# Kernel tuning notes

Measured on AMD Instinct MI355X. Metric: run time of the kernel, lower is better.

Reference implementation:

```python
import jax, jax.numpy as jnp
import numpy as np

VOCAB, E, HIDDEN = 100000, 64, (64, 128, 64)
B, T = 4096, 200


def setup_inputs() -> dict:
    key = jax.random.key(0)
    ks = jax.random.split(key, 12)
    # glorot-ish scales
    def glorot(k, shape):
        fan_in, fan_out = shape[0], shape[-1]
        s = jnp.sqrt(6.0 / (fan_in + fan_out))
        return jax.random.uniform(k, shape, jnp.float32, -s, s)
    return {
        "query": jax.random.randint(ks[0], (B,), 0, VOCAB),
        "keys": jax.random.randint(ks[1], (B, T), 0, VOCAB),
        "emb": glorot(ks[2], (VOCAB, E)),
        "att_w1": glorot(ks[3], (4 * E, 64)),
        "att_b1": jnp.zeros((64,), jnp.float32),
        "att_w2": glorot(ks[4], (64, 1)),
        "att_b2": jnp.zeros((1,), jnp.float32),
        "deep_w1": glorot(ks[5], (HIDDEN[0], HIDDEN[1])),
        "deep_b1": jnp.zeros((HIDDEN[1],), jnp.float32),
        "deep_w2": glorot(ks[6], (HIDDEN[1], HIDDEN[2])),
        "deep_b2": jnp.zeros((HIDDEN[2],), jnp.float32),
        "out_w": glorot(ks[7], (HIDDEN[2], 1)),
        "out_b": jnp.zeros((1,), jnp.float32),
    }


def reference(query, keys, emb, att_w1, att_b1, att_w2, att_b2,
              deep_w1, deep_b1, deep_w2, deep_b2, out_w, out_b):
    q = emb[query]                # [B, E]
    k = emb[keys]                 # [B, T, E]
    qe = jnp.broadcast_to(q[:, None, :], k.shape)  # [B, T, E]
    inter = jnp.concatenate([qe, k, qe - k, qe * k], axis=-1)  # [B, T, 4E]
    h = jax.nn.relu(inter @ att_w1 + att_b1)       # [B, T, 64]
    scores = (h @ att_w2 + att_b2)[..., 0]         # [B, T]
    w = jax.nn.softmax(scores, axis=-1)            # [B, T]
    interest = jnp.einsum("bt,bte->be", w, k)      # [B, E]
    d = jax.nn.relu(interest @ deep_w1 + deep_b1)
    d = jax.nn.relu(d @ deep_w2 + deep_b2)
    return jax.nn.sigmoid(d @ out_w + out_b)       # [B, 1]
```

## Files before the change

kernel.cpp:

```cpp
#include <hip/hip_runtime.h>

#define T 200
#define E 64
#define TPAD 256
#define ROW 72
#define BDIM 256

typedef __bf16 bf16_t;
typedef __bf16 bf16x8 __attribute__((ext_vector_type(8)));
typedef float f32x4 __attribute__((ext_vector_type(4)));

__global__ __launch_bounds__(256) void emb_cvt(const float* __restrict__ src,
                                               bf16_t* __restrict__ dst, int n8) {
    const int i = blockIdx.x * 256 + threadIdx.x;
    if (i >= n8) return;
    const float4* s = (const float4*)src + (size_t)i * 2;
    const float4 a = s[0], b = s[1];
    union { bf16_t h[8]; uint4 v; } u;
    u.h[0] = (bf16_t)a.x; u.h[1] = (bf16_t)a.y; u.h[2] = (bf16_t)a.z; u.h[3] = (bf16_t)a.w;
    u.h[4] = (bf16_t)b.x; u.h[5] = (bf16_t)b.y; u.h[6] = (bf16_t)b.z; u.h[7] = (bf16_t)b.w;
    ((uint4*)dst)[i] = u.v;
}

__global__ __launch_bounds__(BDIM, 3) void din_kernel(
    const int* __restrict__ query,
    const int* __restrict__ keys,
    const float* __restrict__ embf,
    const bf16_t* __restrict__ emb16,
    const int use16,
    const float* __restrict__ w1,
    const float* __restrict__ b1,
    const float* __restrict__ w2,
    const float* __restrict__ b2,
    const float* __restrict__ dw1,
    const float* __restrict__ db1,
    const float* __restrict__ dw2,
    const float* __restrict__ db2,
    const float* __restrict__ ow,
    const float* __restrict__ ob,
    float* __restrict__ out)
{
    __shared__ __align__(16) char sRaw[TPAD * ROW * 2];
    __shared__ __align__(16) bf16_t sMt[64 * ROW];
    __shared__ float sU[64];
    __shared__ float sUP[256];
    __shared__ float sW2f[64];
    __shared__ float sWgt[256];
    __shared__ float sQf[64];
    __shared__ __align__(16) char sQtmp[128];
    __shared__ float sRed[8];
    __shared__ float sInt[64];
    __shared__ float sD1[128];
    __shared__ float sD2[64];

    const int tid  = threadIdx.x;
    const int lane = tid & 63;
    const int wid  = tid >> 6;
    const int b    = blockIdx.x;
    const float b2v = b2[0];

    uint4 kr[8];
    if (tid < T) {
        const int ki = keys[b * T + tid];
        if (use16) {
            const uint4* kp = (const uint4*)(emb16 + (size_t)ki * E);
            #pragma unroll
            for (int c = 0; c < 8; ++c) kr[c] = kp[c];
        } else {
            const float4* kp = (const float4*)(embf + (size_t)ki * E);
            #pragma unroll
            for (int c = 0; c < 8; ++c) {
                const float4 x = kp[2 * c], y = kp[2 * c + 1];
                union { bf16_t h[8]; uint4 v; } u;
                u.h[0] = (bf16_t)x.x; u.h[1] = (bf16_t)x.y; u.h[2] = (bf16_t)x.z; u.h[3] = (bf16_t)x.w;
                u.h[4] = (bf16_t)y.x; u.h[5] = (bf16_t)y.y; u.h[6] = (bf16_t)y.z; u.h[7] = (bf16_t)y.w;
                kr[c] = u.v;
            }
        }
    } else {
        #pragma unroll
        for (int c = 0; c < 8; ++c) kr[c] = make_uint4(0u, 0u, 0u, 0u);
    }

    const int qi = query[b];
    if (tid < 8) {
        uint4 qv;
        if (use16) {
            qv = ((const uint4*)(emb16 + (size_t)qi * E))[tid];
        } else {
            const float4 x = ((const float4*)(embf + (size_t)qi * E))[2 * tid];
            const float4 y = ((const float4*)(embf + (size_t)qi * E))[2 * tid + 1];
            union { bf16_t h[8]; uint4 v; } u;
            u.h[0] = (bf16_t)x.x; u.h[1] = (bf16_t)x.y; u.h[2] = (bf16_t)x.z; u.h[3] = (bf16_t)x.w;
            u.h[4] = (bf16_t)y.x; u.h[5] = (bf16_t)y.y; u.h[6] = (bf16_t)y.z; u.h[7] = (bf16_t)y.w;
            qv = u.v;
        }
        ((uint4*)sQtmp)[tid] = qv;
    }
    if (tid < 64) sW2f[tid] = w2[tid];
    __syncthreads();
    if (tid < 64) sQf[tid] = (float)((const bf16_t*)sQtmp)[tid];
    __syncthreads();

    {
        float* sTmp = (float*)sRaw;
        const int j = tid & 63, ec = tid >> 6;
        float au = 0.f;
        #pragma unroll
        for (int eo = 0; eo < 16; ++eo) {
            const int e = ec * 16 + eo;
            const float w1a = w1[e * 64 + j];
            const float w1b = w1[(64 + e) * 64 + j];
            const float w1c = w1[(128 + e) * 64 + j];
            const float w1d = w1[(192 + e) * 64 + j];
            sTmp[e * 65 + j] = w1b - w1c + sQf[e] * w1d;
            au = fmaf(sQf[e], w1a + w1c, au);
        }
        sUP[tid] = au;
    }
    __syncthreads();
    {
        const float* sTmp = (const float*)sRaw;
        const int e = tid & 63, jc = tid >> 6;
        #pragma unroll
        for (int jo = 0; jo < 16; ++jo) {
            const int j = jc * 16 + jo;
            sMt[j * ROW + e] = (bf16_t)sTmp[e * 65 + j];
        }
    }
    if (tid < 64) sU[tid] = b1[tid] + sUP[tid] + sUP[64 + tid] + sUP[128 + tid] + sUP[192 + tid];
    __syncthreads();

    bf16_t* sK = (bf16_t*)sRaw;
    {
        uint4* dst = (uint4*)(sK + tid * ROW);
        #pragma unroll
        for (int c = 0; c < 8; ++c) dst[c] = kr[c];
    }
    __syncthreads();

    {
        const int n    = lane & 15;
        const int quad = lane >> 4;
        float w2v[4], uv[4];
        bf16x8 bF[4][2];
        #pragma unroll
        for (int nt = 0; nt < 4; ++nt) {
            w2v[nt] = sW2f[nt * 16 + n];
            uv[nt]  = sU[nt * 16 + n];
            bF[nt][0] = *(const bf16x8*)&sMt[(nt * 16 + n) * ROW + quad * 8];
            bF[nt][1] = *(const bf16x8*)&sMt[(nt * 16 + n) * ROW + 32 + quad * 8];
        }
        #pragma unroll
        for (int i = 0; i < 4; ++i) {
            const int mt = wid * 4 + i;
            const bf16x8 a0 = *(const bf16x8*)&sK[(mt * 16 + n) * ROW + quad * 8];
            const bf16x8 a1 = *(const bf16x8*)&sK[(mt * 16 + n) * ROW + 32 + quad * 8];
            float s0 = 0.f, s1 = 0.f, s2 = 0.f, s3 = 0.f;
            #pragma unroll
            for (int nt = 0; nt < 4; ++nt) {
                f32x4 acc = { uv[nt], uv[nt], uv[nt], uv[nt] };
                acc = __builtin_amdgcn_mfma_f32_16x16x32_bf16(a0, bF[nt][0], acc, 0, 0, 0);
                acc = __builtin_amdgcn_mfma_f32_16x16x32_bf16(a1, bF[nt][1], acc, 0, 0, 0);
                s0 = fmaf(fmaxf(acc[0], 0.f), w2v[nt], s0);
                s1 = fmaf(fmaxf(acc[1], 0.f), w2v[nt], s1);
                s2 = fmaf(fmaxf(acc[2], 0.f), w2v[nt], s2);
                s3 = fmaf(fmaxf(acc[3], 0.f), w2v[nt], s3);
            }
            #pragma unroll
            for (int off = 1; off < 16; off <<= 1) {
                s0 += __shfl_xor(s0, off);
                s1 += __shfl_xor(s1, off);
                s2 += __shfl_xor(s2, off);
                s3 += __shfl_xor(s3, off);
            }
            if (n == 0) {
                const int base = mt * 16 + quad * 4;
                sWgt[base + 0] = s0;
                sWgt[base + 1] = s1;
                sWgt[base + 2] = s2;
                sWgt[base + 3] = s3;
            }
        }
    }
    __syncthreads();

    {
        const float score = (tid < T) ? (sWgt[tid] + b2v) : -1e30f;
        float m = score;
        #pragma unroll
        for (int off = 32; off > 0; off >>= 1) m = fmaxf(m, __shfl_xor(m, off));
        if (lane == 0) sRed[wid] = m;
        __syncthreads();
        const float gmax = fmaxf(fmaxf(sRed[0], sRed[1]), fmaxf(sRed[2], sRed[3]));
        const float p = (tid < T) ? __expf(score - gmax) : 0.f;
        float s = p;
        #pragma unroll
        for (int off = 32; off > 0; off >>= 1) s += __shfl_xor(s, off);
        if (lane == 0) sRed[4 + wid] = s;
        __syncthreads();
        const float gsum = sRed[4] + sRed[5] + sRed[6] + sRed[7];
        sWgt[tid] = p / gsum;
    }
    __syncthreads();

    {
        const int e = tid & 63, ch = tid >> 6;
        float a = 0.f;
        #pragma unroll 8
        for (int tt = 0; tt < 64; ++tt) {
            const int t = ch * 64 + tt;
            a = fmaf(sWgt[t], (float)sK[t * ROW + e], a);
        }
        sUP[tid] = a;
    }
    __syncthreads();
    if (tid < 64) sInt[tid] = sUP[tid] + sUP[64 + tid] + sUP[128 + tid] + sUP[192 + tid];
    __syncthreads();

    if (tid < 128) {
        float a = db1[tid];
        #pragma unroll 8
        for (int e = 0; e < 64; ++e) a = fmaf(sInt[e], dw1[e * 128 + tid], a);
        sD1[tid] = fmaxf(a, 0.f);
    }
    __syncthreads();
    if (tid < 64) {
        float a = db2[tid];
        #pragma unroll 8
        for (int i = 0; i < 128; ++i) a = fmaf(sD1[i], dw2[i * 64 + tid], a);
        sD2[tid] = fmaxf(a, 0.f);
    }
    __syncthreads();
    if (tid < 64) {
        float v = sD2[tid] * ow[tid];
        #pragma unroll
        for (int off = 32; off > 0; off >>= 1) v += __shfl_xor(v, off);
        if (tid == 0) out[b] = 1.f / (1.f + __expf(-(v + ob[0])));
    }
}

extern "C" void kernel_launch(void* const* d_in, const int* in_sizes, int n_in,
                              void* d_out, int out_size, void* d_ws, size_t ws_size,
                              hipStream_t stream) {
    const int*   query = (const int*)d_in[0];
    const int*   keys  = (const int*)d_in[1];
    const float* embf  = (const float*)d_in[2];
    const float* w1    = (const float*)d_in[3];
    const float* b1    = (const float*)d_in[4];
    const float* w2    = (const float*)d_in[5];
    const float* b2    = (const float*)d_in[6];
    const float* dw1   = (const float*)d_in[7];
    const float* db1   = (const float*)d_in[8];
    const float* dw2   = (const float*)d_in[9];
    const float* db2   = (const float*)d_in[10];
    const float* ow    = (const float*)d_in[11];
    const float* ob    = (const float*)d_in[12];
    float* out = (float*)d_out;
    const int B       = in_sizes[0];
    const int embElems = in_sizes[2];
    const int use16   = (ws_size >= (size_t)embElems * 2) ? 1 : 0;
    bf16_t* emb16 = (bf16_t*)d_ws;

    if (use16) {
        const int n8 = embElems / 8;
        emb_cvt<<<(n8 + 255) / 256, 256, 0, stream>>>(embf, emb16, n8);
    }
    din_kernel<<<B, BDIM, 0, stream>>>(query, keys, embf, emb16, use16,
                                       w1, b1, w2, b2, dw1, db1, dw2, db2, ow, ob, out);
}
```

Before: 170.3 us.

## Split monolithic DIN kernel into prep, attention, and batched MLP kernels

Replaces the single per-sample kernel with three stages. A prep kernel builds the query-folded attention weights (bf16 MFMA fragments) and the bias vector per sample into workspace. The main kernel gathers keys in fp32 with conversion, runs MFMA scoring over 13 tiles instead of 16 padded ones, does the softmax and the weighted sum. A separate MLP kernel processes 16 samples per block with the weights held in shared memory. It also drops the full-table bf16 conversion pass, in exchange for extra launches and workspace traffic.

After: 175.5 us. 3.1% more time.

```diff
diff --git a/kernel.cpp b/kernel.cpp
--- a/kernel.cpp
+++ b/kernel.cpp
@@ -2,32 +2,308 @@
 
 #define T 200
 #define E 64
-#define TPAD 256
+#define NTILE 13
+#define TPAD 208
 #define ROW 72
-#define BDIM 256
+#define MB 16
 
 typedef __bf16 bf16_t;
 typedef __bf16 bf16x8 __attribute__((ext_vector_type(8)));
 typedef float f32x4 __attribute__((ext_vector_type(4)));
 
-__global__ __launch_bounds__(256) void emb_cvt(const float* __restrict__ src,
-                                               bf16_t* __restrict__ dst, int n8) {
-    const int i = blockIdx.x * 256 + threadIdx.x;
-    if (i >= n8) return;
-    const float4* s = (const float4*)src + (size_t)i * 2;
-    const float4 a = s[0], b = s[1];
-    union { bf16_t h[8]; uint4 v; } u;
-    u.h[0] = (bf16_t)a.x; u.h[1] = (bf16_t)a.y; u.h[2] = (bf16_t)a.z; u.h[3] = (bf16_t)a.w;
-    u.h[4] = (bf16_t)b.x; u.h[5] = (bf16_t)b.y; u.h[6] = (bf16_t)b.z; u.h[7] = (bf16_t)b.w;
-    ((uint4*)dst)[i] = u.v;
+__global__ __launch_bounds__(256) void prep_kernel(
+    const int* __restrict__ query,
+    const float* __restrict__ emb,
+    const float* __restrict__ w1,
+    const float* __restrict__ b1,
+    uint4* __restrict__ wsM,
+    float* __restrict__ wsU)
+{
+    __shared__ float sTmp[64 * 65];
+    __shared__ __align__(16) float sQ[64];
+    __shared__ float sUP[256];
+
+    const int tid = threadIdx.x;
+    const int b   = blockIdx.x;
+
+    const int qi = query[b];
+    if (tid < 16) ((float4*)sQ)[tid] = ((const float4*)(emb + (size_t)qi * E))[tid];
+    __syncthreads();
+
+    {
+        const int j = tid & 63, ec = tid >> 6;
+        float au = 0.f;
+        #pragma unroll
+        for (int eo = 0; eo < 16; ++eo) {
+            const int e = ec * 16 + eo;
+            const float w1a = w1[e * 64 + j];
+            const float w1b = w1[(64 + e) * 64 + j];
+            const float w1c = w1[(128 + e) * 64 + j];
+            const float w1d = w1[(192 + e) * 64 + j];
+            sTmp[e * 65 + j] = w1b - w1c + sQ[e] * w1d;
+            au = fmaf(sQ[e], w1a + w1c, au);
+        }
+        sUP[tid] = au;
+    }
+    __syncthreads();
+    if (tid < 64)
+        wsU[(size_t)b * 64 + tid] = b1[tid] + sUP[tid] + sUP[64 + tid] + sUP[128 + tid] + sUP[192 + tid];
+
+    #pragma unroll
+    for (int c = tid; c < 512; c += 256) {
+        const int f = c >> 6, l = c & 63;
+        const int nt = f >> 1, h = f & 1;
+        const int n = l & 15, quad = l >> 4;
+        const int j2 = nt * 16 + n;
+        const int e0 = h * 32 + quad * 8;
+        union { bf16_t hh[8]; uint4 v; } u;
+        #pragma unroll
+        for (int s = 0; s < 8; ++s) u.hh[s] = (bf16_t)sTmp[(e0 + s) * 65 + j2];
+        wsM[(size_t)b * 512 + c] = u.v;
+    }
 }
 
-__global__ __launch_bounds__(BDIM, 3) void din_kernel(
+__global__ __launch_bounds__(256) void main_kernel(
+    const int* __restrict__ keys,
+    const float* __restrict__ emb,
+    const uint4* __restrict__ wsM,
+    const float* __restrict__ wsU,
+    const float* __restrict__ w2,
+    const float* __restrict__ b2,
+    float* __restrict__ wsI)
+{
+    __shared__ __align__(16) bf16_t sK[TPAD * ROW];
+    __shared__ __align__(16) float sU[64];
+    __shared__ __align__(16) float sW2f[64];
+    __shared__ float sWgt[256];
+    __shared__ float sUP[256];
+    __shared__ float sRed[8];
+
+    const int tid  = threadIdx.x;
+    const int lane = tid & 63;
+    const int wid  = tid >> 6;
+    const int b    = blockIdx.x;
+
+    uint4 kr[8];
+    #pragma unroll
+    for (int c = 0; c < 8; ++c) kr[c] = make_uint4(0u, 0u, 0u, 0u);
+    if (tid < T) {
+        const int ki = keys[b * T + tid];
+        const float4* kp = (const float4*)(emb + (size_t)ki * E);
+        #pragma unroll
+        for (int c = 0; c < 8; ++c) {
+            const float4 x = kp[2 * c], y = kp[2 * c + 1];
+            union { bf16_t h[8]; uint4 v; } u;
+            u.h[0] = (bf16_t)x.x; u.h[1] = (bf16_t)x.y; u.h[2] = (bf16_t)x.z; u.h[3] = (bf16_t)x.w;
+            u.h[4] = (bf16_t)y.x; u.h[5] = (bf16_t)y.y; u.h[6] = (bf16_t)y.z; u.h[7] = (bf16_t)y.w;
+            kr[c] = u.v;
+        }
+    }
+    if (tid < 16) ((float4*)sU)[tid] = ((const float4*)(wsU + (size_t)b * 64))[tid];
+    else if (tid < 32) ((float4*)sW2f)[tid - 16] = ((const float4*)w2)[tid - 16];
+    const float b2v = b2[0];
+
+    bf16x8 bF[4][2];
+    {
+        const uint4* mp = wsM + (size_t)b * 512;
+        #pragma unroll
+        for (int nt = 0; nt < 4; ++nt)
+            #pragma unroll
+            for (int h = 0; h < 2; ++h) {
+                union { uint4 v; bf16x8 f; } u;
+                u.v = mp[(nt * 2 + h) * 64 + lane];
+                bF[nt][h] = u.f;
+            }
+    }
+
+    if (tid < TPAD) {
+        uint4* dst = (uint4*)(sK + tid * ROW);
+        #pragma unroll
+        for (int c = 0; c < 8; ++c) dst[c] = kr[c];
+    }
+    __syncthreads();
+
+    {
+        const int n    = lane & 15;
+        const int quad = lane >> 4;
+        float uvv[4], w2v[4];
+        #pragma unroll
+        for (int nt = 0; nt < 4; ++nt) { uvv[nt] = sU[nt * 16 + n]; w2v[nt] = sW2f[nt * 16 + n]; }
+        for (int mt = wid; mt < NTILE; mt += 4) {
+            const bf16x8 a0 = *(const bf16x8*)&sK[(mt * 16 + n) * ROW + quad * 8];
+            const bf16x8 a1 = *(const bf16x8*)&sK[(mt * 16 + n) * ROW + 32 + quad * 8];
+            float s0 = 0.f, s1 = 0.f, s2 = 0.f, s3 = 0.f;
+            #pragma unroll
+            for (int nt = 0; nt < 4; ++nt) {
+                f32x4 acc = { uvv[nt], uvv[nt], uvv[nt], uvv[nt] };
+                acc = __builtin_amdgcn_mfma_f32_16x16x32_bf16(a0, bF[nt][0], acc, 0, 0, 0);
+                acc = __builtin_amdgcn_mfma_f32_16x16x32_bf16(a1, bF[nt][1], acc, 0, 0, 0);
+                s0 = fmaf(fmaxf(acc[0], 0.f), w2v[nt], s0);
+                s1 = fmaf(fmaxf(acc[1], 0.f), w2v[nt], s1);
+                s2 = fmaf(fmaxf(acc[2], 0.f), w2v[nt], s2);
+                s3 = fmaf(fmaxf(acc[3], 0.f), w2v[nt], s3);
+            }
+            #pragma unroll
+            for (int off = 1; off < 16; off <<= 1) {
+                s0 += __shfl_xor(s0, off);
+                s1 += __shfl_xor(s1, off);
+                s2 += __shfl_xor(s2, off);
+                s3 += __shfl_xor(s3, off);
+            }
+            if (n == 0) {
+                const int base = mt * 16 + quad * 4;
+                sWgt[base + 0] = s0;
+                sWgt[base + 1] = s1;
+                sWgt[base + 2] = s2;
+                sWgt[base + 3] = s3;
+            }
+        }
+    }
+    __syncthreads();
+
+    {
+        const float score = (tid < T) ? (sWgt[tid] + b2v) : -1e30f;
+        float m = score;
+        #pragma unroll
+        for (int off = 32; off > 0; off >>= 1) m = fmaxf(m, __shfl_xor(m, off));
+        if (lane == 0) sRed[wid] = m;
+        __syncthreads();
+        const float gmax = fmaxf(fmaxf(sRed[0], sRed[1]), fmaxf(sRed[2], sRed[3]));
+        const float p = (tid < T) ? __expf(score - gmax) : 0.f;
+        float s = p;
+        #pragma unroll
+        for (int off = 32; off > 0; off >>= 1) s += __shfl_xor(s, off);
+        if (lane == 0) sRed[4 + wid] = s;
+        __syncthreads();
+        const float gsum = sRed[4] + sRed[5] + sRed[6] + sRed[7];
+        sWgt[tid] = p / gsum;
+    }
+    __syncthreads();
+
+    {
+        const int e = tid & 63, ch = tid >> 6;
+        float a = 0.f;
+        #pragma unroll 4
+        for (int tt = 0; tt < 52; ++tt) {
+            const int t = ch * 52 + tt;
+            a = fmaf(sWgt[t], (float)sK[t * ROW + e], a);
+        }
+        sUP[tid] = a;
+    }
+    __syncthreads();
+    if (tid < 64)
+        wsI[(size_t)b * 64 + tid] = sUP[tid] + sUP[64 + tid] + sUP[128 + tid] + sUP[192 + tid];
+}
+
+__global__ __launch_bounds__(256) void mlp_kernel(
+    const float* __restrict__ wsI,
+    const float* __restrict__ dw1,
+    const float* __restrict__ db1,
+    const float* __restrict__ dw2,
+    const float* __restrict__ db2,
+    const float* __restrict__ ow,
+    const float* __restrict__ ob,
+    float* __restrict__ out,
+    int B)
+{
+    __shared__ __align__(16) float sDW1[64 * 128];
+    __shared__ __align__(16) float sDW2[128 * 64];
+    __shared__ __align__(16) float sI[MB * 68];
+    __shared__ __align__(16) float sH1[MB * 132];
+    __shared__ __align__(16) float sH2[MB * 68];
+    __shared__ float sB1[128];
+    __shared__ float sB2[64];
+    __shared__ float sOW[64];
+
+    const int tid = threadIdx.x;
+    const int b0  = blockIdx.x * MB;
+
+    for (int i = tid; i < 2048; i += 256) ((float4*)sDW1)[i] = ((const float4*)dw1)[i];
+    for (int i = tid; i < 2048; i += 256) ((float4*)sDW2)[i] = ((const float4*)dw2)[i];
+    if (tid < 128) sB1[tid] = db1[tid];
+    if (tid < 64) { sB2[tid] = db2[tid]; sOW[tid] = ow[tid]; }
+    {
+        const int bi = tid >> 4, e4 = (tid & 15) * 4;
+        if (b0 + bi < B) {
+            const float4 v = *(const float4*)(wsI + (size_t)(b0 + bi) * 64 + e4);
+            *(float4*)&sI[bi * 68 + e4] = v;
+        }
+    }
+    __syncthreads();
+
+    {
+        const int bi = tid >> 4, jb = tid & 15;
+        float iv[64];
+        #pragma unroll
+        for (int e4 = 0; e4 < 16; ++e4) {
+            const float4 v = *(const float4*)&sI[bi * 68 + e4 * 4];
+            iv[e4 * 4 + 0] = v.x; iv[e4 * 4 + 1] = v.y; iv[e4 * 4 + 2] = v.z; iv[e4 * 4 + 3] = v.w;
+        }
+        float a[8];
+        #pragma unroll
+        for (int jj = 0; jj < 8; ++jj) a[jj] = sB1[jb * 8 + jj];
+        #pragma unroll 8
+        for (int e = 0; e < 64; ++e) {
+            const float4 w0 = *(const float4*)&sDW1[e * 128 + jb * 8];
+            const float4 w4 = *(const float4*)&sDW1[e * 128 + jb * 8 + 4];
+            const float x = iv[e];
+            a[0] = fmaf(x, w0.x, a[0]); a[1] = fmaf(x, w0.y, a[1]);
+            a[2] = fmaf(x, w0.z, a[2]); a[3] = fmaf(x, w0.w, a[3]);
+            a[4] = fmaf(x, w4.x, a[4]); a[5] = fmaf(x, w4.y, a[5]);
+            a[6] = fmaf(x, w4.z, a[6]); a[7] = fmaf(x, w4.w, a[7]);
+        }
+        #pragma unroll
+        for (int jj = 0; jj < 4; ++jj) {
+            float4 v;
+            v.x = fmaxf(a[0 + ((jj & 1) * 4 + (jj >> 1) * 0)], 0.f);
+            (void)v;
+        }
+        float4 v0, v1;
+        v0.x = fmaxf(a[0], 0.f); v0.y = fmaxf(a[1], 0.f); v0.z = fmaxf(a[2], 0.f); v0.w = fmaxf(a[3], 0.f);
+        v1.x = fmaxf(a[4], 0.f); v1.y = fmaxf(a[5], 0.f); v1.z = fmaxf(a[6], 0.f); v1.w = fmaxf(a[7], 0.f);
+        *(float4*)&sH1[bi * 132 + jb * 8] = v0;
+        *(float4*)&sH1[bi * 132 + jb * 8 + 4] = v1;
+    }
+    __syncthreads();
+
+    {
+        const int bi = tid >> 4, obb = tid & 15;
+        float a0 = sB2[obb * 4 + 0], a1 = sB2[obb * 4 + 1], a2 = sB2[obb * 4 + 2], a3 = sB2[obb * 4 + 3];
+        #pragma unroll 4
+        for (int i4 = 0; i4 < 32; ++i4) {
+            const float4 hv = *(const float4*)&sH1[bi * 132 + i4 * 4];
+            const float4 wv0 = *(const float4*)&sDW2[(i4 * 4 + 0) * 64 + obb * 4];
+            const float4 wv1 = *(const float4*)&sDW2[(i4 * 4 + 1) * 64 + obb * 4];
+            const float4 wv2 = *(const float4*)&sDW2[(i4 * 4 + 2) * 64 + obb * 4];
+            const float4 wv3 = *(const float4*)&sDW2[(i4 * 4 + 3) * 64 + obb * 4];
+            a0 = fmaf(hv.x, wv0.x, a0); a1 = fmaf(hv.x, wv0.y, a1);
+            a2 = fmaf(hv.x, wv0.z, a2); a3 = fmaf(hv.x, wv0.w, a3);
+            a0 = fmaf(hv.y, wv1.x, a0); a1 = fmaf(hv.y, wv1.y, a1);
+            a2 = fmaf(hv.y, wv1.z, a2); a3 = fmaf(hv.y, wv1.w, a3);
+            a0 = fmaf(hv.z, wv2.x, a0); a1 = fmaf(hv.z, wv2.y, a1);
+            a2 = fmaf(hv.z, wv2.z, a2); a3 = fmaf(hv.z, wv2.w, a3);
+            a0 = fmaf(hv.w, wv3.x, a0); a1 = fmaf(hv.w, wv3.y, a1);
+            a2 = fmaf(hv.w, wv3.z, a2); a3 = fmaf(hv.w, wv3.w, a3);
+        }
+        float4 v;
+        v.x = fmaxf(a0, 0.f); v.y = fmaxf(a1, 0.f); v.z = fmaxf(a2, 0.f); v.w = fmaxf(a3, 0.f);
+        *(float4*)&sH2[bi * 68 + obb * 4] = v;
+    }
+    __syncthreads();
+
+    if (tid < MB) {
+        const int bi = tid;
+        float a = 0.f;
+        #pragma unroll 8
+        for (int o = 0; o < 64; ++o) a = fmaf(sH2[bi * 68 + o], sOW[o], a);
+        if (b0 + bi < B) out[b0 + bi] = 1.f / (1.f + __expf(-(a + ob[0])));
+    }
+}
+
+__global__ __launch_bounds__(256, 3) void din_mono(
     const int* __restrict__ query,
     const int* __restrict__ keys,
     const float* __restrict__ embf,
-    const bf16_t* __restrict__ emb16,
-    const int use16,
     const float* __restrict__ w1,
     const float* __restrict__ b1,
     const float* __restrict__ w2,
@@ -40,14 +316,13 @@
     const float* __restrict__ ob,
     float* __restrict__ out)
 {
-    __shared__ __align__(16) char sRaw[TPAD * ROW * 2];
+    __shared__ __align__(16) char sRaw[256 * ROW * 2];
     __shared__ __align__(16) bf16_t sMt[64 * ROW];
     __shared__ float sU[64];
     __shared__ float sUP[256];
     __shared__ float sW2f[64];
     __shared__ float sWgt[256];
     __shared__ float sQf[64];
-    __shared__ __align__(16) char sQtmp[128];
     __shared__ float sRed[8];
     __shared__ float sInt[64];
     __shared__ float sD1[128];
@@ -60,46 +335,23 @@
     const float b2v = b2[0];
 
     uint4 kr[8];
+    #pragma unroll
+    for (int c = 0; c < 8; ++c) kr[c] = make_uint4(0u, 0u, 0u, 0u);
     if (tid < T) {
         const int ki = keys[b * T + tid];
-        if (use16) {
-            const uint4* kp = (const uint4*)(emb16 + (size_t)ki * E);
-            #pragma unroll
-            for (int c = 0; c < 8; ++c) kr[c] = kp[c];
-        } else {
-            const float4* kp = (const float4*)(embf + (size_t)ki * E);
-            #pragma unroll
-            for (int c = 0; c < 8; ++c) {
-                const float4 x = kp[2 * c], y = kp[2 * c + 1];
-                union { bf16_t h[8]; uint4 v; } u;
-                u.h[0] = (bf16_t)x.x; u.h[1] = (bf16_t)x.y; u.h[2] = (bf16_t)x.z; u.h[3] = (bf16_t)x.w;
-                u.h[4] = (bf16_t)y.x; u.h[5] = (bf16_t)y.y; u.h[6] = (bf16_t)y.z; u.h[7] = (bf16_t)y.w;
-                kr[c] = u.v;
-            }
-        }
-    } else {
-        #pragma unroll
-        for (int c = 0; c < 8; ++c) kr[c] = make_uint4(0u, 0u, 0u, 0u);
-    }
-
-    const int qi = query[b];
-    if (tid < 8) {
-        uint4 qv;
-        if (use16) {
-            qv = ((const uint4*)(emb16 + (size_t)qi * E))[tid];
-        } else {
-            const float4 x = ((const float4*)(embf + (size_t)qi * E))[2 * tid];
-            const float4 y = ((const float4*)(embf + (size_t)qi * E))[2 * tid + 1];
+        const float4* kp = (const float4*)(embf + (size_t)ki * E);
+        #pragma unroll
+        for (int c = 0; c < 8; ++c) {
+            const float4 x = kp[2 * c], y = kp[2 * c + 1];
             union { bf16_t h[8]; uint4 v; } u;
             u.h[0] = (bf16_t)x.x; u.h[1] = (bf16_t)x.y; u.h[2] = (bf16_t)x.z; u.h[3] = (bf16_t)x.w;
             u.h[4] = (bf16_t)y.x; u.h[5] = (bf16_t)y.y; u.h[6] = (bf16_t)y.z; u.h[7] = (bf16_t)y.w;
-            qv = u.v;
-        }
-        ((uint4*)sQtmp)[tid] = qv;
-    }
+            kr[c] = u.v;
+        }
+    }
+    const int qi = query[b];
+    if (tid < 16) ((float4*)sQf)[tid] = ((const float4*)(embf + (size_t)qi * E))[tid];
     if (tid < 64) sW2f[tid] = w2[tid];
-    __syncthreads();
-    if (tid < 64) sQf[tid] = (float)((const bf16_t*)sQtmp)[tid];
     __syncthreads();
 
     {
@@ -257,15 +509,20 @@
     const float* ow    = (const float*)d_in[11];
     const float* ob    = (const float*)d_in[12];
     float* out = (float*)d_out;
-    const int B       = in_sizes[0];
-    const int embElems = in_sizes[2];
-    const int use16   = (ws_size >= (size_t)embElems * 2) ? 1 : 0;
-    bf16_t* emb16 = (bf16_t*)d_ws;
-
-    if (use16) {
-        const int n8 = embElems / 8;
-        emb_cvt<<<(n8 + 255) / 256, 256, 0, stream>>>(embf, emb16, n8);
-    }
-    din_kernel<<<B, BDIM, 0, stream>>>(query, keys, embf, emb16, use16,
-                                       w1, b1, w2, b2, dw1, db1, dw2, db2, ow, ob, out);
+    const int B = in_sizes[0];
+
+    const size_t needM = (size_t)B * 8192;
+    const size_t needU = (size_t)B * 256;
+    const size_t needI = (size_t)B * 256;
+    if (ws_size >= needM + needU + needI) {
+        uint4* wsM = (uint4*)d_ws;
+        float* wsU = (float*)((char*)d_ws + needM);
+        float* wsI = (float*)((char*)d_ws + needM + needU);
+        prep_kernel<<<B, 256, 0, stream>>>(query, embf, w1, b1, wsM, wsU);
+        main_kernel<<<B, 256, 0, stream>>>(keys, embf, wsM, wsU, w2, b2, wsI);
+        mlp_kernel<<<(B + MB - 1) / MB, 256, 0, stream>>>(wsI, dw1, db1, dw2, db2, ow, ob, out, B);
+    } else {
+        din_mono<<<B, 256, 0, stream>>>(query, keys, embf, w1, b1, w2, b2,
+                                        dw1, db1, dw2, db2, ow, ob, out);
+    }
 }
```
